# Kernel tuning notes

Measured on AMD Instinct MI355X. Metric: run time of the kernel, lower is better.

Reference implementation:

```python
import jax, jax.numpy as jnp
import numpy as np

EPS = 1e-6

def _layernorm(x, gamma, beta):
    mu = jnp.mean(x, axis=-1, keepdims=True)
    var = jnp.mean(jnp.square(x - mu), axis=-1, keepdims=True)
    return (x - mu) * jax.lax.rsqrt(var + EPS) * gamma + beta


def setup_inputs() -> dict:
    key = jax.random.key(0)
    ks = jax.random.split(key, 8)
    B, N, C, F = 2, 2048, 1024, 4096
    s = 0.02
    return {
        "x": jax.random.normal(ks[0], (B, N, C), jnp.float32),
        "Wq": jax.random.normal(ks[1], (C, C), jnp.float32) * s,
        "Wk": jax.random.normal(ks[2], (C, C), jnp.float32) * s,
        "Wv": jax.random.normal(ks[3], (C, C), jnp.float32) * s,
        "Wp": jax.random.normal(ks[4], (C, C), jnp.float32) * s,
        "bp": jnp.zeros((C,), jnp.float32),
        "W1": jax.random.normal(ks[5], (C, F), jnp.float32) * s,
        "b1": jnp.zeros((F,), jnp.float32),
        "W2": jax.random.normal(ks[6], (F, C), jnp.float32) * s,
        "b2": jnp.zeros((C,), jnp.float32),
        "gamma1": jnp.ones((C,), jnp.float32),
        "beta1": jnp.zeros((C,), jnp.float32),
        "gamma2": jnp.ones((C,), jnp.float32),
        "beta2": jnp.zeros((C,), jnp.float32),
    }


def reference(x, Wq, Wk, Wv, Wp, bp, W1, b1, W2, b2, gamma1, beta1, gamma2, beta2):
    B, N, C = x.shape
    H = 16
    D = C // H
    scale = D ** -0.5

    xn = _layernorm(x, gamma1, beta1)
    # QKV projections (no bias); q pre-scaled by head_dim**-0.5 as in source
    q = (xn @ Wq * scale).reshape(B, N, H, D).transpose(0, 2, 1, 3)  # bhnd
    k = (xn @ Wk).reshape(B, N, H, D).transpose(0, 2, 1, 3)
    v = (xn @ Wv).reshape(B, N, H, D).transpose(0, 2, 1, 3)

    attn = jax.nn.softmax(jnp.einsum("bhnd,bhmd->bhnm", q, k), axis=-1)
    y = jnp.einsum("bhnm,bhmd->bhnd", attn, v)
    y = y.transpose(0, 2, 1, 3).reshape(B, N, C)
    x = x + (y @ Wp + bp)

    xn2 = _layernorm(x, gamma2, beta2)
    h = jax.nn.gelu(xn2 @ W1 + b1, approximate=False)  # keras 'gelu' is exact
    x = x + (h @ W2 + b2)
    return x
```

## Files before the change

kernel.cpp:

```cpp
#include <hip/hip_runtime.h>
#include <math.h>

#define BN  4096
#define SEQ 2048
#define CH  1024
#define FF  4096
#define NH  16
#define HD  64

typedef short bf16x8 __attribute__((ext_vector_type(8)));
typedef float f32x4  __attribute__((ext_vector_type(4)));

#define MFMA16(a,b,c) __builtin_amdgcn_mfma_f32_16x16x32_bf16(a,b,c,0,0,0)

__device__ __forceinline__ unsigned short f2b(float f){
  unsigned u = __float_as_uint(f);
  u += 0x7fffu + ((u>>16)&1u);
  return (unsigned short)(u>>16);
}

__device__ __forceinline__ unsigned pk2(float a, float b){
  return __builtin_amdgcn_perm(__float_as_uint(b), __float_as_uint(a), 0x07060302u);
}

#if __has_builtin(__builtin_amdgcn_exp2f)
__device__ __forceinline__ float fexp2(float x){ return __builtin_amdgcn_exp2f(x); }
#else
__device__ __forceinline__ float fexp2(float x){
  float r; asm("v_exp_f32 %0, %1" : "=v"(r) : "v"(x)); return r;
}
#endif

__device__ __forceinline__ void gl2lds16(const void* g, void* l){
  __builtin_amdgcn_global_load_lds(
      (__attribute__((address_space(1))) void*)g,
      (__attribute__((address_space(3))) void*)l, 16, 0, 0);
}

__global__ __launch_bounds__(256) void transpose_all(
    const float* __restrict__ Wq, const float* __restrict__ Wk,
    const float* __restrict__ Wv, const float* __restrict__ Wp,
    const float* __restrict__ W1, const float* __restrict__ W2,
    unsigned short* __restrict__ wq_t, unsigned short* __restrict__ wk_t,
    unsigned short* __restrict__ wv_t, unsigned short* __restrict__ wp_t,
    unsigned short* __restrict__ w1_t, unsigned short* __restrict__ w2_t)
{
  const int id = blockIdx.x;
  const float* in; unsigned short* out; int R, S, bx, by; float scale = 1.f;
  if (id < 1024){
    const int which = id >> 8, sub = id & 255;
    R = CH; S = CH; bx = sub & 15; by = sub >> 4;
    if (which == 0){ in = Wq; out = wq_t; scale = 0.18033688011112042f; }
    else if (which == 1){ in = Wk; out = wk_t; }
    else if (which == 2){ in = Wv; out = wv_t; }
    else               { in = Wp; out = wp_t; }
  } else if (id < 2048){
    const int sub = id - 1024; in = W1; out = w1_t; R = CH; S = FF;
    bx = sub & 63; by = sub >> 6;
  } else {
    const int sub = id - 2048; in = W2; out = w2_t; R = FF; S = CH;
    bx = sub & 15; by = sub >> 4;
  }
  __shared__ float tile[64][65];
  const int tid = threadIdx.x;
  const int tx = tid & 63, ty = tid >> 6;
  const int s0 = bx * 64, r0 = by * 64;
  #pragma unroll
  for (int j = 0; j < 16; j++){
    int r = ty + j*4;
    tile[r][tx] = in[(size_t)(r0 + r)*S + s0 + tx];
  }
  __syncthreads();
  #pragma unroll
  for (int j = 0; j < 16; j++){
    int s = ty + j*4;
    out[(size_t)(s0 + s)*R + r0 + tx] = f2b(tile[tx][s] * scale);
  }
}

__global__ __launch_bounds__(256) void ln_kernel(const float* __restrict__ x,
    const float* __restrict__ gamma, const float* __restrict__ beta,
    unsigned short* __restrict__ out)
{
  const int row = blockIdx.x, tid = threadIdx.x;
  const float4 xv = ((const float4*)(x + (size_t)row*CH))[tid];
  float s  = xv.x + xv.y + xv.z + xv.w;
  float ss = xv.x*xv.x + xv.y*xv.y + xv.z*xv.z + xv.w*xv.w;
  #pragma unroll
  for (int off = 1; off < 64; off <<= 1){
    s  += __shfl_xor(s,  off, 64);
    ss += __shfl_xor(ss, off, 64);
  }
  __shared__ float red[8];
  const int w = tid >> 6;
  if ((tid & 63) == 0){ red[w] = s; red[4+w] = ss; }
  __syncthreads();
  s  = red[0]+red[1]+red[2]+red[3];
  ss = red[4]+red[5]+red[6]+red[7];
  const float mu   = s * (1.f/CH);
  const float rstd = rsqrtf(ss*(1.f/CH) - mu*mu + 1e-6f);
  const float4 g = ((const float4*)gamma)[tid];
  const float4 b = ((const float4*)beta )[tid];
  ushort4 o;
  o.x = f2b((xv.x-mu)*rstd*g.x + b.x);
  o.y = f2b((xv.y-mu)*rstd*g.y + b.y);
  o.z = f2b((xv.z-mu)*rstd*g.z + b.z);
  o.w = f2b((xv.w-mu)*rstd*g.w + b.w);
  ((ushort4*)(out + (size_t)row*CH))[tid] = o;
}

template<int BNT,int BIAS,int GELU,int RES,int OMODE,int SPLITK>
__global__ __launch_bounds__(256,2) void gemm_bt(const unsigned short* __restrict__ A,
    const unsigned short* __restrict__ Bt, const float* __restrict__ bias,
    const float* __restrict__ resid, float* __restrict__ outF,
    unsigned short* __restrict__ outB, unsigned short* __restrict__ outK,
    unsigned short* __restrict__ outV, int M, int Nn, int K)
{
  constexpr int MI = (BNT==128) ? 4 : 2;
  constexpr int BCH = (BNT==128) ? 4 : 2;
  __shared__ __align__(16) unsigned short Al[128*64];
  __shared__ __align__(16) unsigned short Bl[BNT*64];
  const int tid = threadIdx.x;
  const int w = tid >> 6, lane = tid & 63;
  const int quad = lane >> 4, l16 = lane & 15;
  const int m0 = blockIdx.y*128, n0 = blockIdx.x*BNT;
  const int wm = (BNT==128) ? (w >> 1)*64 : w*32;
  const int wn = (BNT==128) ? (w & 1)*64 : 0;
  const int srow = lane >> 3, sslot = lane & 7;
  f32x4 acc[MI][4] = {};
  const int kseg = SPLITK > 1 ? K / SPLITK : K;
  const int kBeg = SPLITK > 1 ? blockIdx.z * kseg : 0;
  for (int k0 = kBeg; k0 < kBeg + kseg; k0 += 64){
    __syncthreads();
    #pragma unroll
    for (int i = 0; i < 4; i++){
      const int rb = (w*4 + i)*8;
      const int r = rb + srow;
      const int c = sslot ^ (r & 7);
      gl2lds16(A + (size_t)(m0 + r)*K + k0 + c*8, (char*)Al + rb*128);
    }
    #pragma unroll
    for (int i = 0; i < BCH; i++){
      const int rb = (w*BCH + i)*8;
      const int r = rb + srow;
      const int c = sslot ^ (r & 7);
      gl2lds16(Bt + (size_t)(n0 + r)*K + k0 + c*8, (char*)Bl + rb*128);
    }
    __syncthreads();
    #pragma unroll
    for (int kc = 0; kc < 2; kc++){
      bf16x8 af[MI], bfr[4];
      #pragma unroll
      for (int mi = 0; mi < MI; mi++){
        const int r = wm + mi*16 + l16;
        af[mi] = *(const bf16x8*)(Al + r*64 + (((kc*4 + quad) ^ (r & 7))*8));
      }
      #pragma unroll
      for (int nj = 0; nj < 4; nj++){
        const int r = wn + nj*16 + l16;
        bfr[nj] = *(const bf16x8*)(Bl + r*64 + (((kc*4 + quad) ^ (r & 7))*8));
      }
      #pragma unroll
      for (int mi = 0; mi < MI; mi++)
        #pragma unroll
        for (int nj = 0; nj < 4; nj++)
          acc[mi][nj] = MFMA16(af[mi], bfr[nj], acc[mi][nj]);
    }
  }
  #pragma unroll
  for (int nj = 0; nj < 4; nj++){
    const int col = n0 + wn + nj*16 + l16;
    const float bv = BIAS ? bias[col] : 0.f;
    #pragma unroll
    for (int mi = 0; mi < MI; mi++){
      #pragma unroll
      for (int r = 0; r < 4; r++){
        const int row = m0 + wm + mi*16 + quad*4 + r;
        float v = acc[mi][nj][r];
        if (SPLITK > 1){
          if (blockIdx.z == 0){
            if (BIAS) v += bias[col];
            if (RES)  v += resid[(size_t)row*Nn + col];
          }
          atomicAdd(&outF[(size_t)row*Nn + col], v);
          continue;
        }
        v += bv;
        if (GELU) v = 0.5f*v*(1.f + erff(v*0.70710678118654752f));
        if (RES)  v += resid[(size_t)row*Nn + col];
        if (OMODE == 0) outF[(size_t)row*Nn + col] = v;
        else if (OMODE == 1) outB[(size_t)row*Nn + col] = f2b(v);
        else {
          const int cg = col >> 10, c = col & (CH-1);
          if (cg == 0)      outB[(size_t)row*CH + c] = f2b(v);
          else if (cg == 1) outK[(size_t)row*CH + c] = f2b(v);
          else {
            const int bb = row >> 11, n = row & (SEQ-1);
            const int hh = c >> 6,  d = c & (HD-1);
            const int np = (n & ~63) | (((n & 15) << 2) | ((n >> 4) & 3));
            outV[((size_t)((bb*NH + hh)*HD + d))*SEQ + np] = f2b(v);
          }
        }
      }
    }
  }
}

__global__ __launch_bounds__(256,2) void attn_kernel(const unsigned short* __restrict__ q,
    const unsigned short* __restrict__ k, const unsigned short* __restrict__ vt,
    unsigned short* __restrict__ y)
{
  __shared__ __align__(16) unsigned short Kl[2][64*64];
  __shared__ __align__(16) unsigned short Vl[2][64*64];
  __shared__ __align__(16) unsigned short Pp[4][64*68];
  const int tid = threadIdx.x;
  const int w = tid >> 6, lane = tid & 63;
  const int wq = w & 1, wk = w >> 1;
  const int quad = lane >> 4, l16 = lane & 15;
  const int bh = blockIdx.y;
  const int b = bh >> 4, h = bh & 15;
  const size_t tb  = ((size_t)b*SEQ)*CH + h*HD;
  const size_t vb_ = (size_t)bh*HD*SEQ;
  const int qr0 = blockIdx.x*128 + wq*64;

  bf16x8 qf[4][2];
  #pragma unroll
  for (int mi = 0; mi < 4; mi++)
    #pragma unroll
    for (int kc = 0; kc < 2; kc++)
      qf[mi][kc] = *(const bf16x8*)(q + tb + (size_t)(qr0 + mi*16 + l16)*CH + kc*32 + quad*8);

  float sacc[4][4];
  f32x4 o[4][4] = {};
  #pragma unroll
  for (int mi = 0; mi < 4; mi++)
    #pragma unroll
    for (int r = 0; r < 4; r++) sacc[mi][r] = 0.f;

  for (int t = 0; t < 16; t++){
    const int kv0 = wk*1024 + t*64;
    __syncthreads();
    #pragma unroll
    for (int i = 0; i < 8; i++){
      const int r = i*8 + (lane >> 3);
      const int c = (lane & 7) ^ (r & 7);
      if (wq == 0)
        gl2lds16(k  + tb  + (size_t)(kv0 + r)*CH + c*8, (char*)&Kl[wk][0] + i*1024);
      else
        gl2lds16(vt + vb_ + (size_t)r*SEQ + kv0 + c*8, (char*)&Vl[wk][0] + i*1024);
    }
    __syncthreads();

    f32x4 s[4][4] = {};
    #pragma unroll
    for (int kc = 0; kc < 2; kc++){
      #pragma unroll
      for (int nj = 0; nj < 4; nj++){
        bf16x8 kf = *(const bf16x8*)(&Kl[wk][0] + (nj*16 + l16)*64 + (((kc*4 + quad) ^ (l16 & 7))*8));
        #pragma unroll
        for (int mi = 0; mi < 4; mi++)
          s[mi][nj] = MFMA16(qf[mi][kc], kf, s[mi][nj]);
      }
    }
    #pragma unroll
    for (int mi = 0; mi < 4; mi++){
      #pragma unroll
      for (int r = 0; r < 4; r++){
        const float p0 = fexp2(s[mi][0][r]);
        const float p1 = fexp2(s[mi][1][r]);
        const float p2 = fexp2(s[mi][2][r]);
        const float p3 = fexp2(s[mi][3][r]);
        sacc[mi][r] += (p0 + p1) + (p2 + p3);
        uint2 pk;
        pk.x = pk2(p0, p1);
        pk.y = pk2(p2, p3);
        const int prow = mi*16 + quad*4 + r;
        *(uint2*)(&Pp[w][prow*68 + l16*4]) = pk;
      }
    }
    #pragma unroll
    for (int kc = 0; kc < 2; kc++){
      bf16x8 pa[4];
      #pragma unroll
      for (int mi = 0; mi < 4; mi++)
        pa[mi] = *(const bf16x8*)(&Pp[w][(mi*16 + l16)*68 + kc*32 + quad*8]);
      #pragma unroll
      for (int nd = 0; nd < 4; nd++){
        bf16x8 vf = *(const bf16x8*)(&Vl[wk][0] + (nd*16 + l16)*64 + (((kc*4 + quad) ^ (l16 & 7))*8));
        #pragma unroll
        for (int mi = 0; mi < 4; mi++)
          o[mi][nd] = MFMA16(pa[mi], vf, o[mi][nd]);
      }
    }
  }

  __syncthreads();
  float* ob = wq ? (float*)&Vl[0][0] : (float*)&Kl[0][0];
  float* sb = (float*)&Pp[2 + wq][0];
  if (wk == 1){
    #pragma unroll
    for (int mi = 0; mi < 4; mi++)
      #pragma unroll
      for (int nd = 0; nd < 4; nd++)
        #pragma unroll
        for (int r = 0; r < 4; r++){
          const int idx = (mi*4 + nd)*4 + r;
          ob[lane*64 + ((idx + lane) & 63)] = o[mi][nd][r];
        }
    #pragma unroll
    for (int mi = 0; mi < 4; mi++)
      #pragma unroll
      for (int r = 0; r < 4; r++)
        sb[lane*16 + ((mi*4 + r + lane) & 15)] = sacc[mi][r];
  }
  __syncthreads();
  if (wk == 0){
    #pragma unroll
    for (int mi = 0; mi < 4; mi++)
      #pragma unroll
      for (int nd = 0; nd < 4; nd++)
        #pragma unroll
        for (int r = 0; r < 4; r++){
          const int idx = (mi*4 + nd)*4 + r;
          o[mi][nd][r] += ob[lane*64 + ((idx + lane) & 63)];
        }
    #pragma unroll
    for (int mi = 0; mi < 4; mi++){
      #pragma unroll
      for (int r = 0; r < 4; r++){
        float sum = sacc[mi][r] + sb[lane*16 + ((mi*4 + r + lane) & 15)];
        #pragma unroll
        for (int off = 1; off < 16; off <<= 1) sum += __shfl_xor(sum, off, 64);
        const float inv = 1.f / sum;
        const int qr = qr0 + mi*16 + quad*4 + r;
        #pragma unroll
        for (int nd = 0; nd < 4; nd++)
          y[tb + (size_t)qr*CH + nd*16 + l16] = f2b(o[mi][nd][r]*inv);
      }
    }
  }
}

extern "C" void kernel_launch(void* const* d_in, const int* in_sizes, int n_in,
                              void* d_out, int out_size, void* d_ws, size_t ws_size,
                              hipStream_t stream)
{
  (void)in_sizes; (void)n_in; (void)out_size; (void)ws_size;
  const float* x   = (const float*)d_in[0];
  const float* Wq  = (const float*)d_in[1];
  const float* Wk  = (const float*)d_in[2];
  const float* Wv  = (const float*)d_in[3];
  const float* Wp  = (const float*)d_in[4];
  const float* bp  = (const float*)d_in[5];
  const float* W1  = (const float*)d_in[6];
  const float* b1  = (const float*)d_in[7];
  const float* W2  = (const float*)d_in[8];
  const float* b2  = (const float*)d_in[9];
  const float* g1  = (const float*)d_in[10];
  const float* be1 = (const float*)d_in[11];
  const float* g2  = (const float*)d_in[12];
  const float* be2 = (const float*)d_in[13];
  float* out = (float*)d_out;
  char* ws = (char*)d_ws;
  const size_t MB = 1024*1024;
  unsigned short* wq_t = (unsigned short*)(ws +  0*MB);
  unsigned short* wk_t = (unsigned short*)(ws +  2*MB);
  unsigned short* wv_t = (unsigned short*)(ws +  4*MB);
  unsigned short* wp_t = (unsigned short*)(ws +  6*MB);
  unsigned short* w1_t = (unsigned short*)(ws +  8*MB);
  unsigned short* w2_t = (unsigned short*)(ws + 16*MB);
  unsigned short* xn   = (unsigned short*)(ws + 24*MB);
  unsigned short* qb   = (unsigned short*)(ws + 32*MB);
  unsigned short* kb   = (unsigned short*)(ws + 40*MB);
  unsigned short* vtb  = (unsigned short*)(ws + 48*MB);
  unsigned short* yb   = (unsigned short*)(ws + 56*MB);
  float*          x2   = (float*)         (ws + 64*MB);
  unsigned short* xn2  = (unsigned short*)(ws + 80*MB);
  unsigned short* hb   = (unsigned short*)(ws + 88*MB);

  transpose_all<<<3072,256,0,stream>>>(Wq, Wk, Wv, Wp, W1, W2,
                                       wq_t, wk_t, wv_t, wp_t, w1_t, w2_t);

  ln_kernel<<<BN,256,0,stream>>>(x, g1, be1, xn);
  gemm_bt<128,0,0,0,3,0><<<dim3(24,32),256,0,stream>>>(xn, wq_t, nullptr, nullptr,
      nullptr, qb, kb, vtb, BN, 3072, CH);
  attn_kernel<<<dim3(16,32),256,0,stream>>>(qb, kb, vtb, yb);
  gemm_bt<64,1,0,1,0,0><<<dim3(16,32),256,0,stream>>>(yb, wp_t, bp, x, x2,
      nullptr, nullptr, nullptr, BN, CH, CH);
  ln_kernel<<<BN,256,0,stream>>>(x2, g2, be2, xn2);
  gemm_bt<128,1,1,0,1,0><<<dim3(32,32),256,0,stream>>>(xn2, w1_t, b1, nullptr, nullptr,
      hb, nullptr, nullptr, BN, FF, CH);
  hipMemsetAsync(out, 0, (size_t)BN*CH*sizeof(float), stream);
  gemm_bt<128,1,0,1,0,4><<<dim3(8,32,4),256,0,stream>>>(hb, w2_t, b2, x2, out,
      nullptr, nullptr, nullptr, BN, CH, FF);
}
```

Baseline: 381.1 us.

## Double-buffer LDS staging in GEMM and retile the FC2 split-K launch

Adds a DBUF template option to the bf16 GEMM. It uses two LDS buffers so the global-to-LDS load of the next K slice is issued before computing the current slice, which cuts one barrier per iteration. This is turned on for the output projection and the FC2 GEMM. FC2 also moves from 128-wide tiles with split-K 4 to 64-wide tiles with split-K 2, keeping the same block count but doing fewer atomic adds per output. The cost is double the LDS per block, which may affect occupancy, and correctness depends on the barrier waiting for the async LDS loads to finish.

```diff
diff --git a/kernel.cpp b/kernel.cpp
--- a/kernel.cpp
+++ b/kernel.cpp
@@ -109,7 +109,7 @@
   ((ushort4*)(out + (size_t)row*CH))[tid] = o;
 }
 
-template<int BNT,int BIAS,int GELU,int RES,int OMODE,int SPLITK>
+template<int BNT,int BIAS,int GELU,int RES,int OMODE,int SPLITK,int DBUF>
 __global__ __launch_bounds__(256,2) void gemm_bt(const unsigned short* __restrict__ A,
     const unsigned short* __restrict__ Bt, const float* __restrict__ bias,
     const float* __restrict__ resid, float* __restrict__ outF,
@@ -118,8 +118,9 @@
 {
   constexpr int MI = (BNT==128) ? 4 : 2;
   constexpr int BCH = (BNT==128) ? 4 : 2;
-  __shared__ __align__(16) unsigned short Al[128*64];
-  __shared__ __align__(16) unsigned short Bl[BNT*64];
+  constexpr int NBUF = DBUF ? 2 : 1;
+  __shared__ __align__(16) unsigned short Al[NBUF][128*64];
+  __shared__ __align__(16) unsigned short Bl[NBUF][BNT*64];
   const int tid = threadIdx.x;
   const int w = tid >> 6, lane = tid & 63;
   const int quad = lane >> 4, l16 = lane & 15;
@@ -130,35 +131,36 @@
   f32x4 acc[MI][4] = {};
   const int kseg = SPLITK > 1 ? K / SPLITK : K;
   const int kBeg = SPLITK > 1 ? blockIdx.z * kseg : 0;
-  for (int k0 = kBeg; k0 < kBeg + kseg; k0 += 64){
-    __syncthreads();
+
+  auto stage = [&](int k0, int bi){
     #pragma unroll
     for (int i = 0; i < 4; i++){
       const int rb = (w*4 + i)*8;
       const int r = rb + srow;
       const int c = sslot ^ (r & 7);
-      gl2lds16(A + (size_t)(m0 + r)*K + k0 + c*8, (char*)Al + rb*128);
+      gl2lds16(A + (size_t)(m0 + r)*K + k0 + c*8, (char*)&Al[bi][0] + rb*128);
     }
     #pragma unroll
     for (int i = 0; i < BCH; i++){
       const int rb = (w*BCH + i)*8;
       const int r = rb + srow;
       const int c = sslot ^ (r & 7);
-      gl2lds16(Bt + (size_t)(n0 + r)*K + k0 + c*8, (char*)Bl + rb*128);
-    }
-    __syncthreads();
+      gl2lds16(Bt + (size_t)(n0 + r)*K + k0 + c*8, (char*)&Bl[bi][0] + rb*128);
+    }
+  };
+  auto compute = [&](int bi){
     #pragma unroll
     for (int kc = 0; kc < 2; kc++){
       bf16x8 af[MI], bfr[4];
       #pragma unroll
       for (int mi = 0; mi < MI; mi++){
         const int r = wm + mi*16 + l16;
-        af[mi] = *(const bf16x8*)(Al + r*64 + (((kc*4 + quad) ^ (r & 7))*8));
+        af[mi] = *(const bf16x8*)(&Al[bi][0] + r*64 + (((kc*4 + quad) ^ (r & 7))*8));
       }
       #pragma unroll
       for (int nj = 0; nj < 4; nj++){
         const int r = wn + nj*16 + l16;
-        bfr[nj] = *(const bf16x8*)(Bl + r*64 + (((kc*4 + quad) ^ (r & 7))*8));
+        bfr[nj] = *(const bf16x8*)(&Bl[bi][0] + r*64 + (((kc*4 + quad) ^ (r & 7))*8));
       }
       #pragma unroll
       for (int mi = 0; mi < MI; mi++)
@@ -166,7 +168,25 @@
         for (int nj = 0; nj < 4; nj++)
           acc[mi][nj] = MFMA16(af[mi], bfr[nj], acc[mi][nj]);
     }
-  }
+  };
+
+  if (DBUF){
+    stage(kBeg, 0);
+    const int S = kseg >> 6;
+    for (int s = 0; s < S; s++){
+      __syncthreads();
+      if (s + 1 < S) stage(kBeg + (s+1)*64, (s+1)&1);
+      compute(s & 1);
+    }
+  } else {
+    for (int k0 = kBeg; k0 < kBeg + kseg; k0 += 64){
+      __syncthreads();
+      stage(k0, 0);
+      __syncthreads();
+      compute(0);
+    }
+  }
+
   #pragma unroll
   for (int nj = 0; nj < 4; nj++){
     const int col = n0 + wn + nj*16 + l16;
@@ -382,15 +402,15 @@
                                        wq_t, wk_t, wv_t, wp_t, w1_t, w2_t);
 
   ln_kernel<<<BN,256,0,stream>>>(x, g1, be1, xn);
-  gemm_bt<128,0,0,0,3,0><<<dim3(24,32),256,0,stream>>>(xn, wq_t, nullptr, nullptr,
+  gemm_bt<128,0,0,0,3,0,0><<<dim3(24,32),256,0,stream>>>(xn, wq_t, nullptr, nullptr,
       nullptr, qb, kb, vtb, BN, 3072, CH);
   attn_kernel<<<dim3(16,32),256,0,stream>>>(qb, kb, vtb, yb);
-  gemm_bt<64,1,0,1,0,0><<<dim3(16,32),256,0,stream>>>(yb, wp_t, bp, x, x2,
+  gemm_bt<64,1,0,1,0,0,1><<<dim3(16,32),256,0,stream>>>(yb, wp_t, bp, x, x2,
       nullptr, nullptr, nullptr, BN, CH, CH);
   ln_kernel<<<BN,256,0,stream>>>(x2, g2, be2, xn2);
-  gemm_bt<128,1,1,0,1,0><<<dim3(32,32),256,0,stream>>>(xn2, w1_t, b1, nullptr, nullptr,
+  gemm_bt<128,1,1,0,1,0,0><<<dim3(32,32),256,0,stream>>>(xn2, w1_t, b1, nullptr, nullptr,
       hb, nullptr, nullptr, BN, FF, CH);
   hipMemsetAsync(out, 0, (size_t)BN*CH*sizeof(float), stream);
-  gemm_bt<128,1,0,1,0,4><<<dim3(8,32,4),256,0,stream>>>(hb, w2_t, b2, x2, out,
+  gemm_bt<64,1,0,1,0,2,1><<<dim3(16,32,2),256,0,stream>>>(hb, w2_t, b2, x2, out,
       nullptr, nullptr, nullptr, BN, CH, FF);
 }
```

After: 378.0 us. Within noise of the previous version (-0.8%).
